# Kernel tuning notes

Hardware: AMD Instinct MI355X
Metric: run time of the kernel (lower is better)

Reference implementation:

```python
import jax, jax.numpy as jnp
import numpy as np

N, E, D = 50000, 800000, 128

def setup_inputs() -> dict:
    key = jax.random.key(0)
    ks = jax.random.split(key, 8)
    x = jax.random.normal(ks[0], (N, D), dtype=jnp.float32)
    edge_index = jax.random.randint(ks[1], (2, E), 0, N, dtype=jnp.int64)
    s2 = 1.0 / np.sqrt(2 * D)
    s4 = 1.0 / np.sqrt(4 * D)
    s1 = 1.0 / np.sqrt(D)
    pre_W = jax.random.uniform(ks[2], (2 * D, D), jnp.float32, -s2, s2)   # pre MLP (1 layer)
    pre_b = jax.random.uniform(ks[3], (D,), jnp.float32, -s2, s2)
    post_W = jax.random.uniform(ks[4], (4 * D, D), jnp.float32, -s4, s4)  # post MLP (1 layer)
    post_b = jax.random.uniform(ks[5], (D,), jnp.float32, -s4, s4)
    lin_W = jax.random.uniform(ks[6], (D, D), jnp.float32, -s1, s1)       # final projection
    lin_b = jax.random.uniform(ks[7], (D,), jnp.float32, -s1, s1)
    return {"x": x, "edge_index": edge_index, "pre_W": pre_W, "pre_b": pre_b,
            "post_W": post_W, "post_b": post_b, "lin_W": lin_W, "lin_b": lin_b}

def reference(x, edge_index, pre_W, pre_b, post_W, post_b, lin_W, lin_b):
    n = x.shape[0]
    src, dst = edge_index[0], edge_index[1]  # message flows src -> dst (source_to_target)
    # message: pre MLP on concat(x_i=target, x_j=source)  [E, 2D] -> [E, D]
    h = jnp.concatenate([x[dst], x[src]], axis=-1)
    m = h @ pre_W + pre_b
    # multi-aggregator scatter: mean, max, sum over destination nodes
    s = jax.ops.segment_sum(m, dst, num_segments=n)
    cnt = jax.ops.segment_sum(jnp.ones((m.shape[0], 1), m.dtype), dst, num_segments=n)
    mean = s / jnp.maximum(cnt, 1.0)
    mx = jax.ops.segment_max(m, dst, num_segments=n)
    mx = jnp.where(cnt > 0, mx, 0.0)  # empty segments -> 0 (PyG fill)
    aggr = jnp.concatenate([mean, mx, s], axis=-1)  # order: mean, max, sum
    # update: post MLP on concat(x, aggr)  [N, 4D] -> [N, D], then final lin
    out = jnp.concatenate([x, aggr], axis=-1) @ post_W + post_b
    out = out @ lin_W + lin_b
    # wrapper: relu + dropout (eval mode -> identity)
    return jax.nn.relu(out)
```

## Files before the change

kernel.cpp:

```cpp
#include <hip/hip_runtime.h>
#include <float.h>

#define NN 50000
#define EE 800000
#define NBKT 196
#define T1 4096
#define CAP2 8192

#define NB_CONV 3125
#define NB_PREP 385
#define NB_CNT  196
#define NB_SETUP (NB_CONV + NB_PREP + NB_CNT)

typedef __attribute__((ext_vector_type(8))) short bf16x8;
typedef __attribute__((ext_vector_type(4))) float f32x4;
typedef unsigned short u16;
typedef unsigned int u32;

__device__ __forceinline__ u16 f2bf(float f) {
  u32 u = __builtin_bit_cast(u32, f);
  u32 r = (u + 0x7fffu + ((u >> 16) & 1u)) >> 16;
  return (u16)r;
}
__device__ __forceinline__ float bflo(u32 q) { return __builtin_bit_cast(float, q << 16); }
__device__ __forceinline__ float bfhi(u32 q) { return __builtin_bit_cast(float, q & 0xffff0000u); }

__global__ __launch_bounds__(256) void k_setup(const float* __restrict__ x,
    const float* __restrict__ post_W, const float* __restrict__ post_b,
    const float* __restrict__ lin_W, const float* __restrict__ lin_b,
    const float* __restrict__ pre_W, const int* __restrict__ ei,
    u16* __restrict__ Xcat, u16* __restrict__ WpT, u16* __restrict__ WpqT,
    float* __restrict__ bp, int* __restrict__ bucket_part) {
  __shared__ int hist[256];
  const int bid = blockIdx.x;
  const int t = threadIdx.x;
  if (bid < NB_CONV) {
    int tid = bid * 256 + t;
    int row = tid >> 4;
    int col = (tid & 15) << 3;
    const float4 v0 = *(const float4*)(x + (size_t)row * 128 + col);
    const float4 v1 = *(const float4*)(x + (size_t)row * 128 + col + 4);
    u16 tmp[8] = {f2bf(v0.x), f2bf(v0.y), f2bf(v0.z), f2bf(v0.w),
                  f2bf(v1.x), f2bf(v1.y), f2bf(v1.z), f2bf(v1.w)};
    *(bf16x8*)(Xcat + (size_t)row * 512 + col) = *(bf16x8*)tmp;
  } else if (bid < NB_CONV + NB_PREP) {
    int idx = (bid - NB_CONV) * 256 + t;
    if (idx < 512 * 128) {
      int i = idx >> 7, j = idx & 127;
      float s = 0.f;
#pragma unroll 8
      for (int c = 0; c < 128; c++) s += post_W[i * 128 + c] * lin_W[c * 128 + j];
      WpT[j * 512 + i] = f2bf(s);
    } else if (idx < 512 * 128 + 256 * 128) {
      int u = idx - 512 * 128;
      int j = u >> 7, k = u & 127;
      float v = (j < 128) ? pre_W[k * 128 + j] : pre_W[(128 + k) * 128 + (j - 128)];
      WpqT[j * 128 + k] = f2bf(v);
    } else if (idx < 512 * 128 + 256 * 128 + 128) {
      int j = idx - (512 * 128 + 256 * 128);
      float s = lin_b[j];
      for (int c = 0; c < 128; c++) s += post_b[c] * lin_W[c * 128 + j];
      bp[j] = s;
    }
  } else {
    int tile = bid - (NB_CONV + NB_PREP);
    hist[t] = 0;
    __syncthreads();
    const int e0 = tile * T1;
    const int ec = min(T1, EE - e0);
    for (int j = t; j < ec; j += 256) atomicAdd(&hist[ei[EE + e0 + j] >> 8], 1);
    __syncthreads();
    bucket_part[tile * 256 + t] = hist[t];
  }
}

__global__ void k_scanbucket(const int* __restrict__ bucket_part,
                             int* __restrict__ bucket_base,
                             int* __restrict__ bucket_cursor) {
  __shared__ int sd[256];
  int t = threadIdx.x;
  int v = 0;
#pragma unroll 4
  for (int b = 0; b < NB_CNT; ++b) v += bucket_part[b * 256 + t];
  sd[t] = v;
  __syncthreads();
  for (int s = 1; s < 256; s <<= 1) {
    int tv = (t >= s) ? sd[t - s] : 0;
    __syncthreads();
    sd[t] += tv;
    __syncthreads();
  }
  int excl = sd[t] - v;
  bucket_base[t] = excl;
  bucket_cursor[t] = excl;
}

__global__ __launch_bounds__(256) void k_bucket(const int* __restrict__ ei,
    int* __restrict__ bucket_cursor, u32* __restrict__ ebuf) {
  __shared__ u32 tilebuf[T1];
  __shared__ u32 gpos[T1];
  __shared__ int hist[256], scan_[256], runbase[256], ctr[256];
  const int t = threadIdx.x;
  const int e0 = blockIdx.x * T1;
  const int ecount = min(T1, EE - e0);
  hist[t] = 0;
  __syncthreads();
  u32 myp[16];
  int myb[16];
#pragma unroll
  for (int k = 0; k < 16; ++k) {
    int idx = t + k * 256;
    myp[k] = 0; myb[k] = 0;
    if (idx < ecount) {
      int e = e0 + idx;
      int s = ei[e], d = ei[EE + e];
      myp[k] = ((u32)d << 16) | (u32)s;
      int b = d >> 8;
      myb[k] = b;
      atomicAdd(&hist[b], 1);
    }
  }
  __syncthreads();
  int v = hist[t];
  scan_[t] = v;
  __syncthreads();
  for (int s_ = 1; s_ < 256; s_ <<= 1) {
    int tv = (t >= s_) ? scan_[t - s_] : 0;
    __syncthreads();
    scan_[t] += tv;
    __syncthreads();
  }
  int excl = scan_[t] - v;
  __syncthreads();
  scan_[t] = excl;
  ctr[t] = 0;
  if (v > 0) runbase[t] = atomicAdd(&bucket_cursor[t], v);
  __syncthreads();
#pragma unroll
  for (int k = 0; k < 16; ++k) {
    int idx = t + k * 256;
    if (idx < ecount) {
      int b = myb[k];
      int l = atomicAdd(&ctr[b], 1);
      int slot = scan_[b] + l;
      tilebuf[slot] = myp[k];
      gpos[slot] = (u32)(runbase[b] + l);
    }
  }
  __syncthreads();
  for (int j = t; j < ecount; j += 256) ebuf[gpos[j]] = tilebuf[j];
}

__global__ __launch_bounds__(256) void k_sortbucket(const u32* __restrict__ ebuf,
    const int* __restrict__ bucket_base, int* __restrict__ row_ptr,
    u16* __restrict__ csr_src) {
  __shared__ u16 sorted[CAP2];
  __shared__ int hist[256], scan_[256], ctr[256];
  const int b = blockIdx.x;
  const int t = threadIdx.x;
  const int base = bucket_base[b];
  const int end = bucket_base[b + 1];
  const int count = end - base;
  hist[t] = 0;
  __syncthreads();
  for (int j = t; j < count; j += 256) atomicAdd(&hist[(ebuf[base + j] >> 16) & 255], 1);
  __syncthreads();
  int v = hist[t];
  scan_[t] = v;
  __syncthreads();
  for (int s_ = 1; s_ < 256; s_ <<= 1) {
    int tv = (t >= s_) ? scan_[t - s_] : 0;
    __syncthreads();
    scan_[t] += tv;
    __syncthreads();
  }
  int excl = scan_[t] - v;
  __syncthreads();
  scan_[t] = excl;
  ctr[t] = 0;
  int node = b * 256 + t;
  if (node < NN) row_ptr[node] = base + excl;
  if (b == NBKT - 1 && t == 0) row_ptr[NN] = EE;
  __syncthreads();
  if (count <= CAP2) {
    for (int j = t; j < count; j += 256) {
      u32 p = ebuf[base + j];
      int ln = (p >> 16) & 255;
      int l = atomicAdd(&ctr[ln], 1);
      sorted[scan_[ln] + l] = (u16)(p & 0xffffu);
    }
    __syncthreads();
    for (int j = t; j < count; j += 256) csr_src[base + j] = sorted[j];
  } else {
    for (int j = t; j < count; j += 256) {
      u32 p = ebuf[base + j];
      int ln = (p >> 16) & 255;
      int l = atomicAdd(&ctr[ln], 1);
      csr_src[base + scan_[ln] + l] = (u16)(p & 0xffffu);
    }
  }
}

template <int KTOT, int LDA, int AROWS>
__device__ __forceinline__ void stage_tiles(const u16* __restrict__ A,
    const u16* __restrict__ BT, int row0, int n0, int k0,
    u16* __restrict__ As, u16* __restrict__ Bs, int t) {
#pragma unroll
  for (int it = 0; it < AROWS / 32; ++it) {
    int c = t + it * 256;
    int row = c >> 3, ch = c & 7;
    int gr = row0 + row;
    bf16x8 v = {};
    if (gr < NN) v = *(const bf16x8*)(A + (size_t)gr * LDA + k0 + (ch << 3));
    *(bf16x8*)(As + row * 64 + ((ch ^ (row & 7)) << 3)) = v;
  }
#pragma unroll
  for (int it = 0; it < 4; ++it) {
    int c = t + it * 256;
    int n = c >> 3, ch = c & 7;
    bf16x8 v = *(const bf16x8*)(BT + (size_t)(n0 + n) * KTOT + k0 + (ch << 3));
    *(bf16x8*)(Bs + n * 64 + ((ch ^ (n & 7)) << 3)) = v;
  }
}

__device__ __forceinline__ bf16x8 ld_frag(const u16* __restrict__ S, int rowbase,
                                          int kk, int lane) {
  int r = rowbase + (lane & 15);
  int chunk = (kk >> 3) + (lane >> 4);
  int sw = chunk ^ (r & 7);
  return *(const bf16x8*)(S + r * 64 + (sw << 3));
}

__global__ __launch_bounds__(256) void k_gemm_pq(const u16* __restrict__ Xcat,
    const u16* __restrict__ WpqT, u16* __restrict__ PQb) {
  __shared__ u16 As[128 * 64];
  __shared__ u16 Bs[128 * 64];
  const int t = threadIdx.x;
  const int lane = t & 63, wid = t >> 6;
  const int wr = wid >> 1, wc = wid & 1;
  const int row0 = blockIdx.x * 128;
  const int n0 = blockIdx.y * 128;
  f32x4 acc[4][4] = {};
  for (int k0 = 0; k0 < 128; k0 += 64) {
    stage_tiles<128, 512, 128>(Xcat, WpqT, row0, n0, k0, As, Bs, t);
    __syncthreads();
#pragma unroll
    for (int kk = 0; kk < 64; kk += 32) {
      bf16x8 af[4], bg[4];
#pragma unroll
      for (int m = 0; m < 4; ++m) af[m] = ld_frag(As, wr * 64 + m * 16, kk, lane);
#pragma unroll
      for (int n = 0; n < 4; ++n) bg[n] = ld_frag(Bs, wc * 64 + n * 16, kk, lane);
#pragma unroll
      for (int m = 0; m < 4; ++m)
#pragma unroll
        for (int n = 0; n < 4; ++n)
          acc[m][n] = __builtin_amdgcn_mfma_f32_16x16x32_bf16(af[m], bg[n], acc[m][n], 0, 0, 0);
    }
    __syncthreads();
  }
#pragma unroll
  for (int m = 0; m < 4; ++m) {
    int rb = row0 + wr * 64 + m * 16 + ((lane >> 4) << 2);
#pragma unroll
    for (int n = 0; n < 4; ++n) {
      int col = n0 + wc * 64 + n * 16 + (lane & 15);
#pragma unroll
      for (int r = 0; r < 4; ++r) {
        int row = rb + r;
        if (row < NN) PQb[(size_t)row * 256 + col] = f2bf(acc[m][n][r]);
      }
    }
  }
}

__global__ __launch_bounds__(256) void k_gemm_out(const u16* __restrict__ Xcat,
    const u16* __restrict__ WpT, const float* __restrict__ bp,
    float* __restrict__ out) {
  __shared__ u16 As[64 * 64];
  __shared__ u16 Bs[128 * 64];
  const int t = threadIdx.x;
  const int lane = t & 63, wid = t >> 6;
  const int wr = wid >> 1, wc = wid & 1;
  const int row0 = blockIdx.x * 64;
  f32x4 acc[2][4] = {};
  for (int k0 = 0; k0 < 512; k0 += 64) {
    stage_tiles<512, 512, 64>(Xcat, WpT, row0, 0, k0, As, Bs, t);
    __syncthreads();
#pragma unroll
    for (int kk = 0; kk < 64; kk += 32) {
      bf16x8 af[2], bg[4];
#pragma unroll
      for (int m = 0; m < 2; ++m) af[m] = ld_frag(As, wr * 32 + m * 16, kk, lane);
#pragma unroll
      for (int n = 0; n < 4; ++n) bg[n] = ld_frag(Bs, wc * 64 + n * 16, kk, lane);
#pragma unroll
      for (int m = 0; m < 2; ++m)
#pragma unroll
        for (int n = 0; n < 4; ++n)
          acc[m][n] = __builtin_amdgcn_mfma_f32_16x16x32_bf16(af[m], bg[n], acc[m][n], 0, 0, 0);
    }
    __syncthreads();
  }
#pragma unroll
  for (int m = 0; m < 2; ++m) {
    int rb = row0 + wr * 32 + m * 16 + ((lane >> 4) << 2);
#pragma unroll
    for (int n = 0; n < 4; ++n) {
      int col = wc * 64 + n * 16 + (lane & 15);
      float bias = bp[col];
#pragma unroll
      for (int r = 0; r < 4; ++r) {
        int row = rb + r;
        if (row < NN) out[(size_t)row * 128 + col] = fmaxf(acc[m][n][r] + bias, 0.f);
      }
    }
  }
}

__global__ __launch_bounds__(256) void k_aggr(const u16* __restrict__ PQb,
    const float* __restrict__ pre_b, const int* __restrict__ row_ptr,
    const u16* __restrict__ csr_src, u16* __restrict__ Xcat) {
  int wid = (blockIdx.x * 256 + threadIdx.x) >> 6;
  int lane = threadIdx.x & 63;
  if (wid >= NN) return;
  int r0 = __builtin_amdgcn_readfirstlane(row_ptr[wid]);
  int r1 = __builtin_amdgcn_readfirstlane(row_ptr[wid + 1]);
  int c = lane * 2;
  const u16* Qbase = PQb + 128 + c;
  float sx = 0.f, sy = 0.f, mxx = -FLT_MAX, mxy = -FLT_MAX;
  int i = r0;
  for (; i + 16 <= r1; i += 16) {
    int s[16];
#pragma unroll
    for (int k = 0; k < 16; ++k) s[k] = __builtin_amdgcn_readfirstlane((int)csr_src[i + k]);
    u32 q[16];
#pragma unroll
    for (int k = 0; k < 16; ++k) q[k] = *(const u32*)(Qbase + (size_t)s[k] * 256);
#pragma unroll
    for (int k = 0; k < 16; ++k) {
      float qx = bflo(q[k]), qy = bfhi(q[k]);
      sx += qx; sy += qy;
      mxx = fmaxf(mxx, qx); mxy = fmaxf(mxy, qy);
    }
  }
  if (i + 8 <= r1) {
    int s[8];
#pragma unroll
    for (int k = 0; k < 8; ++k) s[k] = __builtin_amdgcn_readfirstlane((int)csr_src[i + k]);
    u32 q[8];
#pragma unroll
    for (int k = 0; k < 8; ++k) q[k] = *(const u32*)(Qbase + (size_t)s[k] * 256);
#pragma unroll
    for (int k = 0; k < 8; ++k) {
      float qx = bflo(q[k]), qy = bfhi(q[k]);
      sx += qx; sy += qy;
      mxx = fmaxf(mxx, qx); mxy = fmaxf(mxy, qy);
    }
    i += 8;
  }
  if (i + 4 <= r1) {
    int s[4];
#pragma unroll
    for (int k = 0; k < 4; ++k) s[k] = __builtin_amdgcn_readfirstlane((int)csr_src[i + k]);
    u32 q[4];
#pragma unroll
    for (int k = 0; k < 4; ++k) q[k] = *(const u32*)(Qbase + (size_t)s[k] * 256);
#pragma unroll
    for (int k = 0; k < 4; ++k) {
      float qx = bflo(q[k]), qy = bfhi(q[k]);
      sx += qx; sy += qy;
      mxx = fmaxf(mxx, qx); mxy = fmaxf(mxy, qy);
    }
    i += 4;
  }
  for (; i < r1; ++i) {
    int s = __builtin_amdgcn_readfirstlane((int)csr_src[i]);
    u32 q = *(const u32*)(Qbase + (size_t)s * 256);
    float qx = bflo(q), qy = bfhi(q);
    sx += qx; sy += qy;
    mxx = fmaxf(mxx, qx); mxy = fmaxf(mxy, qy);
  }
  u32 pu = *(const u32*)(PQb + (size_t)wid * 256 + c);
  float2 b = *(const float2*)(pre_b + c);
  float px = bflo(pu) + b.x;
  float py = bfhi(pu) + b.y;
  int deg = r1 - r0;
  float vm_x = 0.f, vm_y = 0.f, vx_x = 0.f, vx_y = 0.f, vs_x = 0.f, vs_y = 0.f;
  if (deg > 0) {
    float inv = 1.0f / (float)deg;
    vm_x = px + sx * inv;          vm_y = py + sy * inv;
    vx_x = px + mxx;               vx_y = py + mxy;
    vs_x = (float)deg * px + sx;   vs_y = (float)deg * py + sy;
  }
  u16* arow = Xcat + (size_t)wid * 512 + 128;
  *(u32*)(arow + c)       = (u32)f2bf(vm_x) | ((u32)f2bf(vm_y) << 16);
  *(u32*)(arow + 128 + c) = (u32)f2bf(vx_x) | ((u32)f2bf(vx_y) << 16);
  *(u32*)(arow + 256 + c) = (u32)f2bf(vs_x) | ((u32)f2bf(vs_y) << 16);
}

extern "C" void kernel_launch(void* const* d_in, const int* in_sizes, int n_in,
                              void* d_out, int out_size, void* d_ws, size_t ws_size,
                              hipStream_t stream) {
  const float* x      = (const float*)d_in[0];
  const int*   ei     = (const int*)d_in[1];
  const float* pre_W  = (const float*)d_in[2];
  const float* pre_b  = (const float*)d_in[3];
  const float* post_W = (const float*)d_in[4];
  const float* post_b = (const float*)d_in[5];
  const float* lin_W  = (const float*)d_in[6];
  const float* lin_b  = (const float*)d_in[7];
  float* out = (float*)d_out;

  char* ws = (char*)d_ws;
  size_t off = 0;
  auto alloc = [&](size_t bytes) { size_t o = off; off = (off + bytes + 511) & ~(size_t)511; return o; };
  u16*   Xcat    = (u16*)(ws + alloc((size_t)NN * 512 * 2));
  u16*   PQb     = (u16*)(ws + alloc((size_t)NN * 256 * 2));
  u16*   WpT     = (u16*)(ws + alloc(128 * 512 * 2));
  u16*   WpqT    = (u16*)(ws + alloc(256 * 128 * 2));
  float* bp      = (float*)(ws + alloc(128 * 4));
  int*   row_ptr = (int*)(ws + alloc((size_t)(NN + 1) * 4));
  int*   bucket_part   = (int*)(ws + alloc((size_t)NB_CNT * 256 * 4));
  int*   bucket_base   = (int*)(ws + alloc(257 * 4));
  int*   bucket_cursor = (int*)(ws + alloc(256 * 4));
  u32*   ebuf    = (u32*)(ws + alloc((size_t)EE * 4));
  u16*   csr_src = (u16*)(ws + alloc((size_t)EE * 2));
  (void)ws_size; (void)in_sizes; (void)n_in; (void)out_size;

  const int NB_M = (NN + 127) / 128;
  const int NB_M64 = (NN + 63) / 64;

  k_setup<<<NB_SETUP, 256, 0, stream>>>(x, post_W, post_b, lin_W, lin_b, pre_W, ei,
                                        Xcat, WpT, WpqT, bp, bucket_part);
  k_scanbucket<<<1, 256, 0, stream>>>(bucket_part, bucket_base, bucket_cursor);
  k_bucket<<<NB_CNT, 256, 0, stream>>>(ei, bucket_cursor, ebuf);
  k_sortbucket<<<NBKT, 256, 0, stream>>>(ebuf, bucket_base, row_ptr, csr_src);
  k_gemm_pq<<<dim3(NB_M, 2), 256, 0, stream>>>(Xcat, WpqT, PQb);
  k_aggr<<<(NN * 64 + 255) / 256, 256, 0, stream>>>(PQb, pre_b, row_ptr, csr_src, Xcat);
  k_gemm_out<<<NB_M64, 256, 0, stream>>>(Xcat, WpT, bp, out);
}
```

Measured before the change: 127.0 us.

## Fuse neighbor aggregation into output GEMM kernel with 128-row tiles

Merges the aggregation kernel and the final GEMM into one kernel. Each 256-thread block first aggregates its own 128 nodes (each wave handles 32 nodes serially), writes them to Xcat, syncs, then runs the GEMM on the same rows with a 128-row tile. This removes a kernel launch and the gap between the two, and the freshly written rows may still be in cache. The cost is much less parallelism for the gather phase: 391 blocks with a serial loop per wave instead of one wave per node, which leaves latency-bound gathers poorly hidden.

```diff
diff --git a/kernel.cpp b/kernel.cpp
--- a/kernel.cpp
+++ b/kernel.cpp
@@ -201,12 +201,12 @@
   }
 }
 
-template <int KTOT, int LDA, int AROWS>
+template <int KTOT, int LDA>
 __device__ __forceinline__ void stage_tiles(const u16* __restrict__ A,
     const u16* __restrict__ BT, int row0, int n0, int k0,
     u16* __restrict__ As, u16* __restrict__ Bs, int t) {
 #pragma unroll
-  for (int it = 0; it < AROWS / 32; ++it) {
+  for (int it = 0; it < 4; ++it) {
     int c = t + it * 256;
     int row = c >> 3, ch = c & 7;
     int gr = row0 + row;
@@ -242,7 +242,7 @@
   const int n0 = blockIdx.y * 128;
   f32x4 acc[4][4] = {};
   for (int k0 = 0; k0 < 128; k0 += 64) {
-    stage_tiles<128, 512, 128>(Xcat, WpqT, row0, n0, k0, As, Bs, t);
+    stage_tiles<128, 512>(Xcat, WpqT, row0, n0, k0, As, Bs, t);
     __syncthreads();
 #pragma unroll
     for (int kk = 0; kk < 64; kk += 32) {
@@ -274,28 +274,112 @@
   }
 }
 
-__global__ __launch_bounds__(256) void k_gemm_out(const u16* __restrict__ Xcat,
+__global__ __launch_bounds__(256) void k_aggr_out(const u16* __restrict__ PQb,
+    const float* __restrict__ pre_b, const int* __restrict__ row_ptr,
+    const u16* __restrict__ csr_src, u16* __restrict__ Xcat,
     const u16* __restrict__ WpT, const float* __restrict__ bp,
     float* __restrict__ out) {
-  __shared__ u16 As[64 * 64];
+  __shared__ u16 As[128 * 64];
   __shared__ u16 Bs[128 * 64];
   const int t = threadIdx.x;
   const int lane = t & 63, wid = t >> 6;
+  const int row0 = blockIdx.x * 128;
+
+  {
+    int c = lane * 2;
+    const u16* Qbase = PQb + 128 + c;
+    for (int j = 0; j < 32; ++j) {
+      int node = row0 + wid * 32 + j;
+      if (node >= NN) break;
+      int r0 = __builtin_amdgcn_readfirstlane(row_ptr[node]);
+      int r1 = __builtin_amdgcn_readfirstlane(row_ptr[node + 1]);
+      float sx = 0.f, sy = 0.f, mxx = -FLT_MAX, mxy = -FLT_MAX;
+      int i = r0;
+      for (; i + 16 <= r1; i += 16) {
+        int s[16];
+#pragma unroll
+        for (int k = 0; k < 16; ++k) s[k] = __builtin_amdgcn_readfirstlane((int)csr_src[i + k]);
+        u32 q[16];
+#pragma unroll
+        for (int k = 0; k < 16; ++k) q[k] = *(const u32*)(Qbase + (size_t)s[k] * 256);
+#pragma unroll
+        for (int k = 0; k < 16; ++k) {
+          float qx = bflo(q[k]), qy = bfhi(q[k]);
+          sx += qx; sy += qy;
+          mxx = fmaxf(mxx, qx); mxy = fmaxf(mxy, qy);
+        }
+      }
+      if (i + 8 <= r1) {
+        int s[8];
+#pragma unroll
+        for (int k = 0; k < 8; ++k) s[k] = __builtin_amdgcn_readfirstlane((int)csr_src[i + k]);
+        u32 q[8];
+#pragma unroll
+        for (int k = 0; k < 8; ++k) q[k] = *(const u32*)(Qbase + (size_t)s[k] * 256);
+#pragma unroll
+        for (int k = 0; k < 8; ++k) {
+          float qx = bflo(q[k]), qy = bfhi(q[k]);
+          sx += qx; sy += qy;
+          mxx = fmaxf(mxx, qx); mxy = fmaxf(mxy, qy);
+        }
+        i += 8;
+      }
+      if (i + 4 <= r1) {
+        int s[4];
+#pragma unroll
+        for (int k = 0; k < 4; ++k) s[k] = __builtin_amdgcn_readfirstlane((int)csr_src[i + k]);
+        u32 q[4];
+#pragma unroll
+        for (int k = 0; k < 4; ++k) q[k] = *(const u32*)(Qbase + (size_t)s[k] * 256);
+#pragma unroll
+        for (int k = 0; k < 4; ++k) {
+          float qx = bflo(q[k]), qy = bfhi(q[k]);
+          sx += qx; sy += qy;
+          mxx = fmaxf(mxx, qx); mxy = fmaxf(mxy, qy);
+        }
+        i += 4;
+      }
+      for (; i < r1; ++i) {
+        int s = __builtin_amdgcn_readfirstlane((int)csr_src[i]);
+        u32 q = *(const u32*)(Qbase + (size_t)s * 256);
+        float qx = bflo(q), qy = bfhi(q);
+        sx += qx; sy += qy;
+        mxx = fmaxf(mxx, qx); mxy = fmaxf(mxy, qy);
+      }
+      u32 pu = *(const u32*)(PQb + (size_t)node * 256 + c);
+      float2 b = *(const float2*)(pre_b + c);
+      float px = bflo(pu) + b.x;
+      float py = bfhi(pu) + b.y;
+      int deg = r1 - r0;
+      float vm_x = 0.f, vm_y = 0.f, vx_x = 0.f, vx_y = 0.f, vs_x = 0.f, vs_y = 0.f;
+      if (deg > 0) {
+        float inv = 1.0f / (float)deg;
+        vm_x = px + sx * inv;          vm_y = py + sy * inv;
+        vx_x = px + mxx;               vx_y = py + mxy;
+        vs_x = (float)deg * px + sx;   vs_y = (float)deg * py + sy;
+      }
+      u16* arow = Xcat + (size_t)node * 512 + 128;
+      *(u32*)(arow + c)       = (u32)f2bf(vm_x) | ((u32)f2bf(vm_y) << 16);
+      *(u32*)(arow + 128 + c) = (u32)f2bf(vx_x) | ((u32)f2bf(vx_y) << 16);
+      *(u32*)(arow + 256 + c) = (u32)f2bf(vs_x) | ((u32)f2bf(vs_y) << 16);
+    }
+  }
+  __syncthreads();
+
   const int wr = wid >> 1, wc = wid & 1;
-  const int row0 = blockIdx.x * 64;
-  f32x4 acc[2][4] = {};
+  f32x4 acc[4][4] = {};
   for (int k0 = 0; k0 < 512; k0 += 64) {
-    stage_tiles<512, 512, 64>(Xcat, WpT, row0, 0, k0, As, Bs, t);
+    stage_tiles<512, 512>(Xcat, WpT, row0, 0, k0, As, Bs, t);
     __syncthreads();
 #pragma unroll
     for (int kk = 0; kk < 64; kk += 32) {
-      bf16x8 af[2], bg[4];
-#pragma unroll
-      for (int m = 0; m < 2; ++m) af[m] = ld_frag(As, wr * 32 + m * 16, kk, lane);
+      bf16x8 af[4], bg[4];
+#pragma unroll
+      for (int m = 0; m < 4; ++m) af[m] = ld_frag(As, wr * 64 + m * 16, kk, lane);
 #pragma unroll
       for (int n = 0; n < 4; ++n) bg[n] = ld_frag(Bs, wc * 64 + n * 16, kk, lane);
 #pragma unroll
-      for (int m = 0; m < 2; ++m)
+      for (int m = 0; m < 4; ++m)
 #pragma unroll
         for (int n = 0; n < 4; ++n)
           acc[m][n] = __builtin_amdgcn_mfma_f32_16x16x32_bf16(af[m], bg[n], acc[m][n], 0, 0, 0);
@@ -303,8 +387,8 @@
     __syncthreads();
   }
 #pragma unroll
-  for (int m = 0; m < 2; ++m) {
-    int rb = row0 + wr * 32 + m * 16 + ((lane >> 4) << 2);
+  for (int m = 0; m < 4; ++m) {
+    int rb = row0 + wr * 64 + m * 16 + ((lane >> 4) << 2);
 #pragma unroll
     for (int n = 0; n < 4; ++n) {
       int col = wc * 64 + n * 16 + (lane & 15);
@@ -316,87 +400,6 @@
       }
     }
   }
-}
-
-__global__ __launch_bounds__(256) void k_aggr(const u16* __restrict__ PQb,
-    const float* __restrict__ pre_b, const int* __restrict__ row_ptr,
-    const u16* __restrict__ csr_src, u16* __restrict__ Xcat) {
-  int wid = (blockIdx.x * 256 + threadIdx.x) >> 6;
-  int lane = threadIdx.x & 63;
-  if (wid >= NN) return;
-  int r0 = __builtin_amdgcn_readfirstlane(row_ptr[wid]);
-  int r1 = __builtin_amdgcn_readfirstlane(row_ptr[wid + 1]);
-  int c = lane * 2;
-  const u16* Qbase = PQb + 128 + c;
-  float sx = 0.f, sy = 0.f, mxx = -FLT_MAX, mxy = -FLT_MAX;
-  int i = r0;
-  for (; i + 16 <= r1; i += 16) {
-    int s[16];
-#pragma unroll
-    for (int k = 0; k < 16; ++k) s[k] = __builtin_amdgcn_readfirstlane((int)csr_src[i + k]);
-    u32 q[16];
-#pragma unroll
-    for (int k = 0; k < 16; ++k) q[k] = *(const u32*)(Qbase + (size_t)s[k] * 256);
-#pragma unroll
-    for (int k = 0; k < 16; ++k) {
-      float qx = bflo(q[k]), qy = bfhi(q[k]);
-      sx += qx; sy += qy;
-      mxx = fmaxf(mxx, qx); mxy = fmaxf(mxy, qy);
-    }
-  }
-  if (i + 8 <= r1) {
-    int s[8];
-#pragma unroll
-    for (int k = 0; k < 8; ++k) s[k] = __builtin_amdgcn_readfirstlane((int)csr_src[i + k]);
-    u32 q[8];
-#pragma unroll
-    for (int k = 0; k < 8; ++k) q[k] = *(const u32*)(Qbase + (size_t)s[k] * 256);
-#pragma unroll
-    for (int k = 0; k < 8; ++k) {
-      float qx = bflo(q[k]), qy = bfhi(q[k]);
-      sx += qx; sy += qy;
-      mxx = fmaxf(mxx, qx); mxy = fmaxf(mxy, qy);
-    }
-    i += 8;
-  }
-  if (i + 4 <= r1) {
-    int s[4];
-#pragma unroll
-    for (int k = 0; k < 4; ++k) s[k] = __builtin_amdgcn_readfirstlane((int)csr_src[i + k]);
-    u32 q[4];
-#pragma unroll
-    for (int k = 0; k < 4; ++k) q[k] = *(const u32*)(Qbase + (size_t)s[k] * 256);
-#pragma unroll
-    for (int k = 0; k < 4; ++k) {
-      float qx = bflo(q[k]), qy = bfhi(q[k]);
-      sx += qx; sy += qy;
-      mxx = fmaxf(mxx, qx); mxy = fmaxf(mxy, qy);
-    }
-    i += 4;
-  }
-  for (; i < r1; ++i) {
-    int s = __builtin_amdgcn_readfirstlane((int)csr_src[i]);
-    u32 q = *(const u32*)(Qbase + (size_t)s * 256);
-    float qx = bflo(q), qy = bfhi(q);
-    sx += qx; sy += qy;
-    mxx = fmaxf(mxx, qx); mxy = fmaxf(mxy, qy);
-  }
-  u32 pu = *(const u32*)(PQb + (size_t)wid * 256 + c);
-  float2 b = *(const float2*)(pre_b + c);
-  float px = bflo(pu) + b.x;
-  float py = bfhi(pu) + b.y;
-  int deg = r1 - r0;
-  float vm_x = 0.f, vm_y = 0.f, vx_x = 0.f, vx_y = 0.f, vs_x = 0.f, vs_y = 0.f;
-  if (deg > 0) {
-    float inv = 1.0f / (float)deg;
-    vm_x = px + sx * inv;          vm_y = py + sy * inv;
-    vx_x = px + mxx;               vx_y = py + mxy;
-    vs_x = (float)deg * px + sx;   vs_y = (float)deg * py + sy;
-  }
-  u16* arow = Xcat + (size_t)wid * 512 + 128;
-  *(u32*)(arow + c)       = (u32)f2bf(vm_x) | ((u32)f2bf(vm_y) << 16);
-  *(u32*)(arow + 128 + c) = (u32)f2bf(vx_x) | ((u32)f2bf(vx_y) << 16);
-  *(u32*)(arow + 256 + c) = (u32)f2bf(vs_x) | ((u32)f2bf(vs_y) << 16);
 }
 
 extern "C" void kernel_launch(void* const* d_in, const int* in_sizes, int n_in,
@@ -429,7 +432,6 @@
   (void)ws_size; (void)in_sizes; (void)n_in; (void)out_size;
 
   const int NB_M = (NN + 127) / 128;
-  const int NB_M64 = (NN + 63) / 64;
 
   k_setup<<<NB_SETUP, 256, 0, stream>>>(x, post_W, post_b, lin_W, lin_b, pre_W, ei,
                                         Xcat, WpT, WpqT, bp, bucket_part);
@@ -437,6 +439,5 @@
   k_bucket<<<NB_CNT, 256, 0, stream>>>(ei, bucket_cursor, ebuf);
   k_sortbucket<<<NBKT, 256, 0, stream>>>(ebuf, bucket_base, row_ptr, csr_src);
   k_gemm_pq<<<dim3(NB_M, 2), 256, 0, stream>>>(Xcat, WpqT, PQb);
-  k_aggr<<<(NN * 64 + 255) / 256, 256, 0, stream>>>(PQb, pre_b, row_ptr, csr_src, Xcat);
-  k_gemm_out<<<NB_M64, 256, 0, stream>>>(Xcat, WpT, bp, out);
-}
+  k_aggr_out<<<NB_M, 256, 0, stream>>>(PQb, pre_b, row_ptr, csr_src, Xcat, WpT, bp, out);
+}
```

New measurement: 188.6 us. +48.5%, slower.
